# Kernel tuning notes

Measured on AMD Instinct MI355X. Metric: run time of the kernel, lower is better.

Reference implementation:

```python
import jax, jax.numpy as jnp
import numpy as np

KH, KW = 3, 3
STRIDE, PAD, DIL = 1, 1, 1


def setup_inputs() -> dict:
    key = jax.random.key(0)
    k1, k2, k3 = jax.random.split(key, 3)
    B, C, H, W = 4, 128, 128, 128
    O = 128
    x = jax.random.normal(k1, (B, C, H, W), dtype=jnp.float32)
    # torchvision layout: [B, 2*K, Ho, Wo], per kernel tap (dy, dx) interleaved
    offset = jax.random.normal(k2, (B, 2 * KH * KW, H, W), dtype=jnp.float32)
    weight = jax.random.normal(k3, (O, C, KH, KW), dtype=jnp.float32) * 0.05
    return {"x": x, "offset": offset, "weight": weight}


def _deform_conv2d(x, offset, weight):
    B, C, H, W = x.shape
    O = weight.shape[0]
    K = KH * KW
    Ho = (H + 2 * PAD - DIL * (KH - 1) - 1) // STRIDE + 1
    Wo = (W + 2 * PAD - DIL * (KW - 1) - 1) // STRIDE + 1

    # base sampling grid: p = stride*(h,w) - pad + dil*(ki,kj) + offset
    ky = jnp.arange(KH, dtype=x.dtype) * DIL - PAD            # [-1, 0, 1]
    kx = jnp.arange(KW, dtype=x.dtype) * DIL - PAD
    kyy = jnp.repeat(ky, KW)                                   # [K] row-major
    kxx = jnp.tile(kx, KH)                                     # [K]
    gh = jnp.arange(Ho, dtype=x.dtype) * STRIDE                # [Ho]
    gw = jnp.arange(Wo, dtype=x.dtype) * STRIDE                # [Wo]

    off = offset.reshape(B, K, 2, Ho, Wo)
    oy, ox = off[:, :, 0], off[:, :, 1]                        # [B,K,Ho,Wo]
    py = gh[None, None, :, None] + kyy[None, :, None, None] + oy
    px = gw[None, None, None, :] + kxx[None, :, None, None] + ox

    y0 = jnp.floor(py).astype(jnp.int32)
    x0 = jnp.floor(px).astype(jnp.int32)
    y1, x1 = y0 + 1, x0 + 1
    wy = py - y0.astype(x.dtype)                               # [B,K,Ho,Wo]
    wx = px - x0.astype(x.dtype)

    xf = x.reshape(B, C, H * W)

    def gather(yi, xi):
        # zero padding outside the image (torchvision semantics)
        valid = (yi >= 0) & (yi < H) & (xi >= 0) & (xi < W)
        idx = jnp.clip(yi, 0, H - 1) * W + jnp.clip(xi, 0, W - 1)
        g = jax.vmap(lambda xb, ib: xb[:, ib])(xf, idx.reshape(B, -1))
        g = g.reshape(B, C, K, Ho, Wo)
        return g * valid[:, None].astype(x.dtype)

    one = jnp.asarray(1, x.dtype)
    w00 = ((one - wy) * (one - wx))[:, None]                   # [B,1,K,Ho,Wo]
    w01 = ((one - wy) * wx)[:, None]
    w10 = (wy * (one - wx))[:, None]
    w11 = (wy * wx)[:, None]
    patches = (w00 * gather(y0, x0) + w01 * gather(y0, x1)
               + w10 * gather(y1, x0) + w11 * gather(y1, x1))  # [B,C,K,Ho,Wo]

    wmat = weight.reshape(O, C, K)                             # row-major taps match offset order
    return jnp.einsum('bckhw,ock->bohw', patches, wmat)


def reference(x, offset, weight):
    return _deform_conv2d(x, offset, weight)
```

## Files before the change

### kernel.cpp

```cpp
#include <hip/hip_runtime.h>
#include <hip/hip_bf16.h>
#include <stdint.h>

#define B_   4
#define C_   128
#define H_   128
#define W_   128
#define O_   128
#define HW_  16384
#define KK   9
#define KD   1152
#define TM   32
#define PS_LD 1160

typedef float f32x4 __attribute__((ext_vector_type(4)));
typedef short s16x8 __attribute__((ext_vector_type(8)));
typedef uint32_t u32x4 __attribute__((ext_vector_type(4)));

__device__ __forceinline__ uint32_t f2bf(float f) {
  uint32_t u = __builtin_bit_cast(uint32_t, f);
  u += 0x7FFFu + ((u >> 16) & 1u);
  return u >> 16;
}
__device__ __forceinline__ float bflo(uint32_t v) { return __builtin_bit_cast(float, v << 16); }
__device__ __forceinline__ float bfhi(uint32_t v) { return __builtin_bit_cast(float, v & 0xFFFF0000u); }
__device__ __forceinline__ uint32_t pk2bf(float lo, float hi) {
  return f2bf(lo) | (f2bf(hi) << 16);
}

__global__ __launch_bounds__(256) void k_transpose(const float* __restrict__ x,
                                                   uint16_t* __restrict__ xt) {
  __shared__ uint32_t upk[64][33];
  int tid = threadIdx.x;
  int bid = blockIdx.x;
  int b   = bid >> 9;
  int r   = bid & 511;
  int c0  = (r >> 8) << 6;
  int hw0 = (r & 255) << 6;

#pragma unroll
  for (int p = 0; p < 2; ++p) {
    int cp = p * 16 + (tid >> 4);
    int c  = c0 + (cp << 1);
    int hw = (tid & 15) << 2;
    const float* s0 = x + ((size_t)(b * C_ + c) * HW_) + hw0 + hw;
    f32x4 v0 = *reinterpret_cast<const f32x4*>(s0);
    f32x4 v1 = *reinterpret_cast<const f32x4*>(s0 + HW_);
#pragma unroll
    for (int q = 0; q < 4; ++q)
      upk[hw + q][cp] = pk2bf(v0[q], v1[q]);
  }
  __syncthreads();
#pragma unroll
  for (int p = 0; p < 2; ++p) {
    int hwl = p * 32 + (tid >> 3);
    int j   = tid & 7;
    u32x4 o;
#pragma unroll
    for (int i = 0; i < 4; ++i) o[i] = upk[hwl][j * 4 + i];
    *reinterpret_cast<u32x4*>(xt + ((size_t)(b * HW_ + hw0 + hwl) * C_) + c0 + j * 8) = o;
  }
}

__global__ __launch_bounds__(256) void k_weight(const float* __restrict__ w,
                                                uint16_t* __restrict__ wt) {
  int g = blockIdx.x * 256 + threadIdx.x;
  int o   = g / KD;
  int rem = g - o * KD;
  int kp  = rem >> 7;
  int c   = rem & 127;
  wt[g] = (uint16_t)f2bf(w[(o * C_ + c) * KK + kp]);
}

__global__ __launch_bounds__(512, 4) void k_main(const float* __restrict__ off,
                                                 const uint16_t* __restrict__ xt,
                                                 const uint16_t* __restrict__ wt,
                                                 float* __restrict__ out) {
  __shared__ __align__(16) unsigned char smem[TM * PS_LD * 2];
  uint16_t (*ps)[PS_LD] = reinterpret_cast<uint16_t(*)[PS_LD]>(smem);

  int tid  = threadIdx.x;
  int lane = tid & 63, wv = tid >> 6;

  int sbid = ((blockIdx.x & 7) << 8) + (blockIdx.x >> 3);
  int p0   = sbid * TM;
  int b    = p0 >> 14;
  int hw0  = p0 & (HW_ - 1);

  {
    int q  = lane >> 4;
    int j  = lane & 15;
    int pix = (wv << 2) + q;
    int hw  = hw0 + pix;
    int h = hw >> 7, w = hw & 127;
    int c0 = j << 3;
    const uint16_t* bbase = xt + (size_t)b * HW_ * C_ + c0;
    const float*    offb  = off + (size_t)b * 18 * HW_ + hw;
    uint16_t*       psW   = &ps[pix][c0];

#pragma unroll
    for (int k = 0; k < KK; ++k) {
      const int kdy = k / 3 - 1, kdx = k % 3 - 1;
      float oy = offb[(2 * k) * HW_];
      float ox = offb[(2 * k + 1) * HW_];
      float py = (float)(h + kdy) + oy;
      float px = (float)(w + kdx) + ox;
      float yf = floorf(py), xf = floorf(px);
      float wy = py - yf, wx = px - xf;
      int y0 = (int)yf, x0 = (int)xf;
      int y1 = y0 + 1, x1 = x0 + 1;
      int y0c = min(max(y0, 0), H_ - 1), y1c = min(max(y1, 0), H_ - 1);
      int x0c = min(max(x0, 0), W_ - 1), x1c = min(max(x1, 0), W_ - 1);
      bool vy0 = (unsigned)y0 < (unsigned)H_, vy1 = (unsigned)y1 < (unsigned)H_;
      bool vx0 = (unsigned)x0 < (unsigned)W_, vx1 = (unsigned)x1 < (unsigned)W_;
      float ay = 1.f - wy, ax = 1.f - wx;
      float w00 = (vy0 && vx0) ? ay * ax : 0.f;
      float w01 = (vy0 && vx1) ? ay * wx : 0.f;
      float w10 = (vy1 && vx0) ? wy * ax : 0.f;
      float w11 = (vy1 && vx1) ? wy * wx : 0.f;

      u32x4 g00 = *reinterpret_cast<const u32x4*>(bbase + (((y0c << 7) + x0c) << 7));
      u32x4 g01 = *reinterpret_cast<const u32x4*>(bbase + (((y0c << 7) + x1c) << 7));
      u32x4 g10 = *reinterpret_cast<const u32x4*>(bbase + (((y1c << 7) + x0c) << 7));
      u32x4 g11 = *reinterpret_cast<const u32x4*>(bbase + (((y1c << 7) + x1c) << 7));

      u32x4 outv;
#pragma unroll
      for (int i = 0; i < 4; ++i) {
        float lo = w00 * bflo(g00[i]) + w01 * bflo(g01[i]) + w10 * bflo(g10[i]) + w11 * bflo(g11[i]);
        float hi = w00 * bfhi(g00[i]) + w01 * bfhi(g01[i]) + w10 * bfhi(g10[i]) + w11 * bfhi(g11[i]);
        outv[i] = pk2bf(lo, hi);
      }
      *reinterpret_cast<u32x4*>(psW + (k << 7)) = outv;
    }
  }
  __syncthreads();

  f32x4 acc0 = {0.f, 0.f, 0.f, 0.f}, acc1 = {0.f, 0.f, 0.f, 0.f};
  {
    int r = lane & 15, g = lane >> 4;
    const uint16_t* wrow = wt + (wv * 16 + r) * KD + g * 8;
    const uint16_t* a0p  = &ps[r][g * 8];
    const uint16_t* a1p  = &ps[16 + r][g * 8];
#pragma unroll
    for (int s = 0; s < 36; ++s) {
      s16x8 bf = *reinterpret_cast<const s16x8*>(wrow + s * 32);
      s16x8 a0 = *reinterpret_cast<const s16x8*>(a0p + s * 32);
      s16x8 a1 = *reinterpret_cast<const s16x8*>(a1p + s * 32);
      acc0 = __builtin_amdgcn_mfma_f32_16x16x32_bf16(a0, bf, acc0, 0, 0, 0);
      acc1 = __builtin_amdgcn_mfma_f32_16x16x32_bf16(a1, bf, acc1, 0, 0, 0);
    }
  }
  __syncthreads();

  float* lout = reinterpret_cast<float*>(smem);
  {
    int r = lane & 15, g = lane >> 4;
    int o = wv * 16 + r;
#pragma unroll
    for (int i = 0; i < 4; ++i) lout[o * 33 + (g << 2) + i] = acc0[i];
#pragma unroll
    for (int i = 0; i < 4; ++i) lout[o * 33 + 16 + (g << 2) + i] = acc1[i];
  }
  __syncthreads();
  {
    int pl = tid & 31, og = tid >> 5;
    float* obase = out + (b * O_) * HW_ + hw0 + pl;
#pragma unroll
    for (int i = 0; i < 8; ++i) {
      int o = og * 8 + i;
      obase[o * HW_] = lout[o * 33 + pl];
    }
  }
}

extern "C" void kernel_launch(void* const* d_in, const int* in_sizes, int n_in,
                              void* d_out, int out_size, void* d_ws, size_t ws_size,
                              hipStream_t stream) {
  const float* x   = (const float*)d_in[0];
  const float* off = (const float*)d_in[1];
  const float* wgt = (const float*)d_in[2];
  float* out = (float*)d_out;

  uint16_t* xt = (uint16_t*)d_ws;
  uint16_t* wt = xt + (size_t)B_ * HW_ * C_;

  k_transpose<<<2048, 256, 0, stream>>>(x, xt);
  k_weight<<<576, 256, 0, stream>>>(wgt, wt);
  k_main<<<2048, 512, 0, stream>>>(off, xt, wt, out);
}
```

Before: 184.7 us.

## Double-buffer per-tap patch tiles in LDS to overlap gather with MFMA

Replaces the single-pass design, which gathered and interpolated all 9 taps into a large LDS patch matrix before running the GEMM, with a per-tap software pipeline. Each tap's bilinear samples go into one of two small LDS buffers. The gather loads for tap k+1 and the offset prefetch are issued before the MFMAs for tap k, and the interpolation is written afterwards. LDS per block drops from about 74KB to about 17KB, and the launch bounds allow more resident blocks. The cost is a barrier per tap and higher register pressure from prefetched offsets and in-flight gather data.

```diff
diff --git a/kernel.cpp b/kernel.cpp
--- a/kernel.cpp
+++ b/kernel.cpp
@@ -11,7 +11,7 @@
 #define KK   9
 #define KD   1152
 #define TM   32
-#define PS_LD 1160
+#define CLD  136
 
 typedef float f32x4 __attribute__((ext_vector_type(4)));
 typedef short s16x8 __attribute__((ext_vector_type(8)));
@@ -47,115 +47,134 @@
     f32x4 v0 = *reinterpret_cast<const f32x4*>(s0);
     f32x4 v1 = *reinterpret_cast<const f32x4*>(s0 + HW_);
 #pragma unroll
-    for (int q = 0; q < 4; ++q)
-      upk[hw + q][cp] = pk2bf(v0[q], v1[q]);
+    for (int qq = 0; qq < 4; ++qq)
+      upk[hw + qq][cp] = pk2bf(v0[qq], v1[qq]);
   }
   __syncthreads();
 #pragma unroll
   for (int p = 0; p < 2; ++p) {
     int hwl = p * 32 + (tid >> 3);
-    int j   = tid & 7;
+    int jj  = tid & 7;
     u32x4 o;
 #pragma unroll
-    for (int i = 0; i < 4; ++i) o[i] = upk[hwl][j * 4 + i];
-    *reinterpret_cast<u32x4*>(xt + ((size_t)(b * HW_ + hw0 + hwl) * C_) + c0 + j * 8) = o;
+    for (int i = 0; i < 4; ++i) o[i] = upk[hwl][jj * 4 + i];
+    *reinterpret_cast<u32x4*>(xt + ((size_t)(b * HW_ + hw0 + hwl) * C_) + c0 + jj * 8) = o;
   }
 }
 
 __global__ __launch_bounds__(256) void k_weight(const float* __restrict__ w,
                                                 uint16_t* __restrict__ wt) {
-  int g = blockIdx.x * 256 + threadIdx.x;
-  int o   = g / KD;
-  int rem = g - o * KD;
+  int gg = blockIdx.x * 256 + threadIdx.x;
+  int o   = gg / KD;
+  int rem = gg - o * KD;
   int kp  = rem >> 7;
   int c   = rem & 127;
-  wt[g] = (uint16_t)f2bf(w[(o * C_ + c) * KK + kp]);
-}
-
-__global__ __launch_bounds__(512, 4) void k_main(const float* __restrict__ off,
+  wt[gg] = (uint16_t)f2bf(w[(o * C_ + c) * KK + kp]);
+}
+
+__global__ __launch_bounds__(512, 8) void k_main(const float* __restrict__ off,
                                                  const uint16_t* __restrict__ xt,
                                                  const uint16_t* __restrict__ wt,
                                                  float* __restrict__ out) {
-  __shared__ __align__(16) unsigned char smem[TM * PS_LD * 2];
-  uint16_t (*ps)[PS_LD] = reinterpret_cast<uint16_t(*)[PS_LD]>(smem);
-
+  __shared__ __align__(16) uint16_t ps2[2][TM][CLD];
   int tid  = threadIdx.x;
   int lane = tid & 63, wv = tid >> 6;
 
-  int sbid = ((blockIdx.x & 7) << 8) + (blockIdx.x >> 3);
+  int sbid = ((blockIdx.x & 7) << 8) | (blockIdx.x >> 3);
   int p0   = sbid * TM;
   int b    = p0 >> 14;
   int hw0  = p0 & (HW_ - 1);
 
+  int q   = lane >> 4;
+  int j   = lane & 15;
+  int pix = (wv << 2) + q;
+  int hw  = hw0 + pix;
+  int h = hw >> 7, w = hw & 127;
+  uint32_t cb = (uint32_t)(j << 4);
+  const char*  xtb  = (const char*)(xt + (size_t)b * HW_ * C_);
+  const float* offb = off + (size_t)b * 18 * HW_ + hw;
+
+  int r = lane & 15, g = lane >> 4;
+  const uint16_t* wrow = wt + (wv * 16 + r) * KD + g * 8;
+
+  f32x4 acc0 = {0.f,0.f,0.f,0.f}, acc1 = {0.f,0.f,0.f,0.f};
+
+  float oyv[9], oxv[9];
+  u32x4 g0, g1, g2, g3;
+  float w00, w01, w10, w11;
+
+#define GATHER_TAP(K)                                                          \
+  {                                                                            \
+    const int kdy = (K)/3 - 1, kdx = (K)%3 - 1;                                \
+    float py = (float)(h + kdy) + oyv[K];                                      \
+    float px = (float)(w + kdx) + oxv[K];                                      \
+    float yf = floorf(py), xf = floorf(px);                                    \
+    float wy = py - yf, wx = px - xf;                                          \
+    int y0 = (int)yf, x0 = (int)xf;                                            \
+    int y1 = y0 + 1, x1 = x0 + 1;                                              \
+    int y0c = min(max(y0,0),H_-1), y1c = min(max(y1,0),H_-1);                  \
+    int x0c = min(max(x0,0),W_-1), x1c = min(max(x1,0),W_-1);                  \
+    bool vy0 = (unsigned)y0 < (unsigned)H_, vy1 = (unsigned)y1 < (unsigned)H_; \
+    bool vx0 = (unsigned)x0 < (unsigned)W_, vx1 = (unsigned)x1 < (unsigned)W_; \
+    float ay = 1.f - wy, ax = 1.f - wx;                                        \
+    w00 = (vy0 && vx0) ? ay*ax : 0.f;                                          \
+    w01 = (vy0 && vx1) ? ay*wx : 0.f;                                          \
+    w10 = (vy1 && vx0) ? wy*ax : 0.f;                                          \
+    w11 = (vy1 && vx1) ? wy*wx : 0.f;                                          \
+    uint32_t o00 = ((uint32_t)((y0c<<7)+x0c)<<8) + cb;                         \
+    uint32_t o01 = ((uint32_t)((y0c<<7)+x1c)<<8) + cb;                         \
+    uint32_t o10 = ((uint32_t)((y1c<<7)+x0c)<<8) + cb;                         \
+    uint32_t o11 = ((uint32_t)((y1c<<7)+x1c)<<8) + cb;                         \
+    g0 = *reinterpret_cast<const u32x4*>(xtb + o00);                           \
+    g1 = *reinterpret_cast<const u32x4*>(xtb + o01);                           \
+    g2 = *reinterpret_cast<const u32x4*>(xtb + o10);                           \
+    g3 = *reinterpret_cast<const u32x4*>(xtb + o11);                           \
+  }
+
+#define INTERP_TAP(BUF)                                                        \
+  {                                                                            \
+    u32x4 ov;                                                                  \
+    _Pragma("unroll")                                                          \
+    for (int i = 0; i < 4; ++i) {                                              \
+      float lo = w00*bflo(g0[i]) + w01*bflo(g1[i]) + w10*bflo(g2[i]) + w11*bflo(g3[i]); \
+      float hi = w00*bfhi(g0[i]) + w01*bfhi(g1[i]) + w10*bfhi(g2[i]) + w11*bfhi(g3[i]); \
+      ov[i] = pk2bf(lo, hi);                                                   \
+    }                                                                          \
+    *reinterpret_cast<u32x4*>(&ps2[BUF][pix][j*8]) = ov;                       \
+  }
+
+  oyv[0] = offb[0];        oxv[0] = offb[HW_];
+  oyv[1] = offb[2*HW_];    oxv[1] = offb[3*HW_];
+  oyv[2] = offb[4*HW_];    oxv[2] = offb[5*HW_];
+  GATHER_TAP(0);
+  INTERP_TAP(0);
+  __syncthreads();
+
+#pragma unroll
+  for (int k = 0; k < 9; ++k) {
+    if (k < 8) GATHER_TAP(k+1);
+    if (k < 6) {
+      oyv[k+3] = offb[(2*(k+3))*HW_];
+      oxv[k+3] = offb[(2*(k+3)+1)*HW_];
+    }
+    {
+      const uint16_t* b0 = &ps2[k&1][r][g*8];
+      const uint16_t* b1 = &ps2[k&1][16+r][g*8];
+#pragma unroll
+      for (int s = 0; s < 4; ++s) {
+        s16x8 bfv = *reinterpret_cast<const s16x8*>(wrow + (k*4+s)*32);
+        s16x8 a0  = *reinterpret_cast<const s16x8*>(b0 + s*32);
+        s16x8 a1  = *reinterpret_cast<const s16x8*>(b1 + s*32);
+        acc0 = __builtin_amdgcn_mfma_f32_16x16x32_bf16(a0, bfv, acc0, 0,0,0);
+        acc1 = __builtin_amdgcn_mfma_f32_16x16x32_bf16(a1, bfv, acc1, 0,0,0);
+      }
+    }
+    if (k < 8) INTERP_TAP((k+1)&1);
+    __syncthreads();
+  }
+
+  float* lout = reinterpret_cast<float*>(&ps2[0][0][0]);
   {
-    int q  = lane >> 4;
-    int j  = lane & 15;
-    int pix = (wv << 2) + q;
-    int hw  = hw0 + pix;
-    int h = hw >> 7, w = hw & 127;
-    int c0 = j << 3;
-    const uint16_t* bbase = xt + (size_t)b * HW_ * C_ + c0;
-    const float*    offb  = off + (size_t)b * 18 * HW_ + hw;
-    uint16_t*       psW   = &ps[pix][c0];
-
-#pragma unroll
-    for (int k = 0; k < KK; ++k) {
-      const int kdy = k / 3 - 1, kdx = k % 3 - 1;
-      float oy = offb[(2 * k) * HW_];
-      float ox = offb[(2 * k + 1) * HW_];
-      float py = (float)(h + kdy) + oy;
-      float px = (float)(w + kdx) + ox;
-      float yf = floorf(py), xf = floorf(px);
-      float wy = py - yf, wx = px - xf;
-      int y0 = (int)yf, x0 = (int)xf;
-      int y1 = y0 + 1, x1 = x0 + 1;
-      int y0c = min(max(y0, 0), H_ - 1), y1c = min(max(y1, 0), H_ - 1);
-      int x0c = min(max(x0, 0), W_ - 1), x1c = min(max(x1, 0), W_ - 1);
-      bool vy0 = (unsigned)y0 < (unsigned)H_, vy1 = (unsigned)y1 < (unsigned)H_;
-      bool vx0 = (unsigned)x0 < (unsigned)W_, vx1 = (unsigned)x1 < (unsigned)W_;
-      float ay = 1.f - wy, ax = 1.f - wx;
-      float w00 = (vy0 && vx0) ? ay * ax : 0.f;
-      float w01 = (vy0 && vx1) ? ay * wx : 0.f;
-      float w10 = (vy1 && vx0) ? wy * ax : 0.f;
-      float w11 = (vy1 && vx1) ? wy * wx : 0.f;
-
-      u32x4 g00 = *reinterpret_cast<const u32x4*>(bbase + (((y0c << 7) + x0c) << 7));
-      u32x4 g01 = *reinterpret_cast<const u32x4*>(bbase + (((y0c << 7) + x1c) << 7));
-      u32x4 g10 = *reinterpret_cast<const u32x4*>(bbase + (((y1c << 7) + x0c) << 7));
-      u32x4 g11 = *reinterpret_cast<const u32x4*>(bbase + (((y1c << 7) + x1c) << 7));
-
-      u32x4 outv;
-#pragma unroll
-      for (int i = 0; i < 4; ++i) {
-        float lo = w00 * bflo(g00[i]) + w01 * bflo(g01[i]) + w10 * bflo(g10[i]) + w11 * bflo(g11[i]);
-        float hi = w00 * bfhi(g00[i]) + w01 * bfhi(g01[i]) + w10 * bfhi(g10[i]) + w11 * bfhi(g11[i]);
-        outv[i] = pk2bf(lo, hi);
-      }
-      *reinterpret_cast<u32x4*>(psW + (k << 7)) = outv;
-    }
-  }
-  __syncthreads();
-
-  f32x4 acc0 = {0.f, 0.f, 0.f, 0.f}, acc1 = {0.f, 0.f, 0.f, 0.f};
-  {
-    int r = lane & 15, g = lane >> 4;
-    const uint16_t* wrow = wt + (wv * 16 + r) * KD + g * 8;
-    const uint16_t* a0p  = &ps[r][g * 8];
-    const uint16_t* a1p  = &ps[16 + r][g * 8];
-#pragma unroll
-    for (int s = 0; s < 36; ++s) {
-      s16x8 bf = *reinterpret_cast<const s16x8*>(wrow + s * 32);
-      s16x8 a0 = *reinterpret_cast<const s16x8*>(a0p + s * 32);
-      s16x8 a1 = *reinterpret_cast<const s16x8*>(a1p + s * 32);
-      acc0 = __builtin_amdgcn_mfma_f32_16x16x32_bf16(a0, bf, acc0, 0, 0, 0);
-      acc1 = __builtin_amdgcn_mfma_f32_16x16x32_bf16(a1, bf, acc1, 0, 0, 0);
-    }
-  }
-  __syncthreads();
-
-  float* lout = reinterpret_cast<float*>(smem);
-  {
-    int r = lane & 15, g = lane >> 4;
     int o = wv * 16 + r;
 #pragma unroll
     for (int i = 0; i < 4; ++i) lout[o * 33 + (g << 2) + i] = acc0[i];
@@ -165,13 +184,15 @@
   __syncthreads();
   {
     int pl = tid & 31, og = tid >> 5;
-    float* obase = out + (b * O_) * HW_ + hw0 + pl;
+    float* obase = out + (size_t)(b * O_) * HW_ + hw0 + pl;
 #pragma unroll
     for (int i = 0; i < 8; ++i) {
       int o = og * 8 + i;
-      obase[o * HW_] = lout[o * 33 + pl];
+      obase[(size_t)o * HW_] = lout[o * 33 + pl];
     }
   }
+#undef GATHER_TAP
+#undef INTERP_TAP
 }
 
 extern "C" void kernel_launch(void* const* d_in, const int* in_sizes, int n_in,
```

Result: faster. 176.5 us (-4.5%).
